# Kernel tuning notes

Measured on AMD Instinct MI355X. Metric: run time of the kernel, lower is better.

## Reference

```python
import jax, jax.numpy as jnp
import numpy as np

B, T, D, H, E = 32, 512, 768, 12, 6  # batch, seq(=input_size), n_embd, num_heads, per-head dim
DFF = 4 * D
EPS = 1e-5


def setup_inputs() -> dict:
    key = jax.random.key(0)
    ks = jax.random.split(key, 10)
    s = 0.02
    return {
        "x": jax.random.normal(ks[0], (B, T, D), jnp.float32),
        "Wq": jax.random.normal(ks[1], (H, D, E), jnp.float32) * s,
        "Wk": jax.random.normal(ks[2], (H, D, E), jnp.float32) * s,
        "Wv": jax.random.normal(ks[3], (H, D, E), jnp.float32) * s,
        "Wo": jax.random.normal(ks[4], (H * E, D), jnp.float32) * s,
        "bo": jnp.zeros((D,), jnp.float32),
        "W1": jax.random.normal(ks[5], (D, DFF), jnp.float32) * s,
        "b1": jnp.zeros((DFF,), jnp.float32),
        "W2": jax.random.normal(ks[6], (DFF, D), jnp.float32) * s,
        "b2": jnp.zeros((D,), jnp.float32),
        "g1": jnp.ones((D,), jnp.float32),
        "beta1": jnp.zeros((D,), jnp.float32),
        "g2": jnp.ones((D,), jnp.float32),
        "beta2": jnp.zeros((D,), jnp.float32),
    }


def _layernorm(x, g, b):
    m = jnp.mean(x, axis=-1, keepdims=True)
    v = jnp.var(x, axis=-1, keepdims=True)  # biased, matches torch LayerNorm
    return (x - m) * jax.lax.rsqrt(v + EPS) * g + b


def reference(x, Wq, Wk, Wv, Wo, bo, W1, b1, W2, b2, g1, beta1, g2, beta2):
    # --- pre-LN multi-head causal attention (dropout = identity, eval mode) ---
    xn = _layernorm(x, g1, beta1)
    q = jnp.einsum("btd,hde->bhte", xn, Wq)
    k = jnp.einsum("btd,hde->bhte", xn, Wk)
    v = jnp.einsum("btd,hde->bhte", xn, Wv)
    scores = jnp.einsum("bhte,bhse->bhts", q, k) * (E ** -0.5)
    causal = jnp.tril(jnp.ones((T, T), dtype=bool))
    scores = jnp.where(causal, scores, -jnp.inf)
    w = jax.nn.softmax(scores, axis=-1)
    o = jnp.einsum("bhts,bhse->bhte", w, v)
    o = o.transpose(0, 2, 1, 3).reshape(B, T, H * E)  # concat heads -> [B,T,72]
    x = x + o @ Wo + bo
    # --- pre-LN feed-forward ---
    y = _layernorm(x, g2, beta2)
    ff = jax.nn.relu(y @ W1 + b1) @ W2 + b2
    return x + ff
```

## Files before the change

### kernel.cpp

```cpp
#include <hip/hip_runtime.h>
#include <hip/hip_bf16.h>

#define BT 16384
#define DIM 768
#define NH 12
#define DFF 3072

typedef __attribute__((ext_vector_type(8))) short short8;
typedef __attribute__((ext_vector_type(4))) float floatx4;
typedef __attribute__((ext_vector_type(4))) unsigned short ushort4b;

using bf16 = __hip_bfloat16;

static __device__ __forceinline__ float b2f(bf16 v) { return __bfloat162float(v); }
static __device__ __forceinline__ bf16 f2b(float v) { return __float2bfloat16(v); }

static __device__ __forceinline__ void gload_lds16(const void* g, void* l) {
    __builtin_amdgcn_global_load_lds(
        (const __attribute__((address_space(1))) unsigned int*)g,
        (__attribute__((address_space(3))) unsigned int*)l, 16, 0, 0);
}

__global__ __launch_bounds__(256) void pack_small_kernel(
    const float* __restrict__ Wq, const float* __restrict__ Wk, const float* __restrict__ Wv,
    const float* __restrict__ Wo, bf16* __restrict__ wqkv, bf16* __restrict__ wo_t)
{
    int i = blockIdx.x * 256 + threadIdx.x;
    const int S0 = 256 * 768, S1 = 768 * 96;
    if (i < S0) {
        int c = i / 768, dd = i % 768;
        float v = 0.f;
        if (c < 216) {
            int sel = c / 72, cc = c % 72, h = cc / 6, e = cc % 6;
            const float* W = (sel == 0) ? Wq : (sel == 1) ? Wk : Wv;
            v = W[((size_t)h * 768 + dd) * 6 + e];
        }
        wqkv[i] = f2b(v);
    } else if ((i -= S0) < S1) {
        int n = i / 96, r = i % 96;
        wo_t[i] = f2b(r < 72 ? Wo[r * 768 + n] : 0.f);
    }
}

__global__ __launch_bounds__(256) void transpose_kernel(
    const float* __restrict__ in, bf16* __restrict__ out, int R, int C)
{
    __shared__ float t[32][33];
    int c0 = blockIdx.x * 32, r0 = blockIdx.y * 32;
    int cx = threadIdx.x & 31, ry = threadIdx.x >> 5;
#pragma unroll
    for (int j = 0; j < 4; j++)
        t[ry + j * 8][cx] = in[(size_t)(r0 + ry + j * 8) * C + c0 + cx];
    __syncthreads();
    int rx = cx, cy = ry;
#pragma unroll
    for (int j = 0; j < 4; j++)
        out[(size_t)(c0 + cy + j * 8) * R + r0 + rx] = f2b(t[rx][cy + j * 8]);
}

__global__ __launch_bounds__(192) void ln_kernel(
    const float* __restrict__ x, const float* __restrict__ g, const float* __restrict__ be,
    bf16* __restrict__ out)
{
    int row = blockIdx.x;
    int tid = threadIdx.x;
    const float4* xr = (const float4*)(x + (size_t)row * DIM);
    float4 v = xr[tid];
    float s = v.x + v.y + v.z + v.w;
    float s2 = v.x * v.x + v.y * v.y + v.z * v.z + v.w * v.w;
#pragma unroll
    for (int off = 32; off; off >>= 1) {
        s += __shfl_down(s, off);
        s2 += __shfl_down(s2, off);
    }
    __shared__ float red[6];
    int wv = tid >> 6, ln = tid & 63;
    if (ln == 0) { red[wv] = s; red[3 + wv] = s2; }
    __syncthreads();
    float ts = red[0] + red[1] + red[2];
    float ts2 = red[3] + red[4] + red[5];
    float mean = ts * (1.f / 768.f);
    float var = ts2 * (1.f / 768.f) - mean * mean;
    float rstd = rsqrtf(var + 1e-5f);
    int c = tid * 4;
    float o0 = (v.x - mean) * rstd * g[c + 0] + be[c + 0];
    float o1 = (v.y - mean) * rstd * g[c + 1] + be[c + 1];
    float o2 = (v.z - mean) * rstd * g[c + 2] + be[c + 2];
    float o3 = (v.w - mean) * rstd * g[c + 3] + be[c + 3];
    bf16 h0 = f2b(o0), h1 = f2b(o1), h2 = f2b(o2), h3 = f2b(o3);
    ushort4b pk;
    pk[0] = *(unsigned short*)&h0; pk[1] = *(unsigned short*)&h1;
    pk[2] = *(unsigned short*)&h2; pk[3] = *(unsigned short*)&h3;
    *(ushort4b*)(out + (size_t)row * DIM + c) = pk;
}

template <int NSLAB, bool RELU, bool BIAS, bool RES, bool BF16OUT>
__global__ __launch_bounds__(256) void gemm_kernel(
    const bf16* __restrict__ A, const bf16* __restrict__ Bt,
    const float* __restrict__ bias, const float* __restrict__ res,
    void* __restrict__ Cv, int M, int N, int K)
{
    constexpr int SMEM_BYTES = BF16OUT ? (128 * 136 * 2) : (NSLAB * 2 * 128 * 32 * 2);
    __shared__ __align__(16) char smem[SMEM_BYTES];
    bf16* lA = (bf16*)smem;
    bf16* lB = lA + NSLAB * 128 * 32;

    const int tid = threadIdx.x;
    const int bm = blockIdx.x * 128;
    const int bn = blockIdx.y * 128;
    const int wave = tid >> 6, lane = tid & 63;
    const int wm = (wave >> 1) * 64, wn = (wave & 1) * 64;
    const int quad = lane >> 4, l16 = lane & 15;
    const int lrow = lane >> 2;
    const int lkc = (lane & 3) * 8;

    floatx4 acc[4][4] = {};

    for (int k0 = 0; k0 < K; k0 += NSLAB * 32) {
#pragma unroll
        for (int s = 0; s < NSLAB; s++) {
#pragma unroll
            for (int it = 0; it < 2; it++) {
                int r = wave * 32 + it * 16;
                gload_lds16(A + (size_t)(bm + r + lrow) * K + k0 + s * 32 + lkc,
                            lA + s * 4096 + r * 32);
                gload_lds16(Bt + (size_t)(bn + r + lrow) * K + k0 + s * 32 + lkc,
                            lB + s * 4096 + r * 32);
            }
        }
        __syncthreads();
#pragma unroll
        for (int s = 0; s < NSLAB; s++) {
            short8 af[4], bfr[4];
#pragma unroll
            for (int mt = 0; mt < 4; mt++)
                af[mt] = *(const short8*)(lA + s * 4096 + (wm + mt * 16 + l16) * 32 + quad * 8);
#pragma unroll
            for (int nt = 0; nt < 4; nt++)
                bfr[nt] = *(const short8*)(lB + s * 4096 + (wn + nt * 16 + l16) * 32 + quad * 8);
#pragma unroll
            for (int mt = 0; mt < 4; mt++)
#pragma unroll
                for (int nt = 0; nt < 4; nt++)
                    acc[mt][nt] = __builtin_amdgcn_mfma_f32_16x16x32_bf16(af[mt], bfr[nt], acc[mt][nt], 0, 0, 0);
        }
        __syncthreads();
    }

    if constexpr (BF16OUT) {
        bf16* ltile = (bf16*)smem;
#pragma unroll
        for (int mt = 0; mt < 4; mt++) {
#pragma unroll
            for (int nt = 0; nt < 4; nt++) {
                int tc = wn + nt * 16 + l16;
#pragma unroll
                for (int r = 0; r < 4; r++) {
                    int tr = wm + mt * 16 + quad * 4 + r;
                    float v0 = acc[mt][nt][r];
                    if constexpr (BIAS) v0 += bias[bn + tc];
                    if constexpr (RELU) v0 = fmaxf(v0, 0.f);
                    ltile[tr * 136 + tc] = f2b(v0);
                }
            }
        }
        __syncthreads();
        bf16* C = (bf16*)Cv;
        int rr0 = tid >> 4, col8 = (tid & 15) * 8;
        int gc = bn + col8;
#pragma unroll
        for (int p = 0; p < 8; p++) {
            int rr = p * 16 + rr0;
            if (gc < N)
                *(short8*)(C + (size_t)(bm + rr) * N + gc) =
                    *(const short8*)(ltile + rr * 136 + col8);
        }
    } else {
        float* C = (float*)Cv;
#pragma unroll
        for (int mt = 0; mt < 4; mt++) {
#pragma unroll
            for (int nt = 0; nt < 4; nt++) {
                int gc = bn + wn + nt * 16 + l16;
                if (gc < N) {
#pragma unroll
                    for (int r = 0; r < 4; r++) {
                        int gr = bm + wm + mt * 16 + quad * 4 + r;
                        float v0 = acc[mt][nt][r];
                        if constexpr (BIAS) v0 += bias[gc];
                        if constexpr (RES) v0 += res[(size_t)gr * N + gc];
                        if constexpr (RELU) v0 = fmaxf(v0, 0.f);
                        C[(size_t)gr * N + gc] = v0;
                    }
                }
            }
        }
    }
}

template <int NTC, int TPB, bool RELU, bool BIAS, bool RES, bool BF16OUT>
__global__ __launch_bounds__(512, 2) void gemm192_kernel(
    const bf16* __restrict__ A, const bf16* __restrict__ Bt,
    const float* __restrict__ bias, const float* __restrict__ res,
    void* __restrict__ Cv, int N)
{
    constexpr int KC = NTC * 64;
    constexpr int NG = NTC * TPB;
    extern __shared__ __align__(16) char smem[];

    const int sid = ((blockIdx.x & 7) << 5) + (blockIdx.x >> 3);
    const int bm = (sid & 63) << 8;
    const int bnBase = (sid >> 6) * (TPB * 192);

    const int tid = threadIdx.x;
    const int w = tid >> 6, lane = tid & 63;
    const int wm = w >> 1, wn = w & 1;
    const int l16 = lane & 15, quad = lane >> 4;

    const int rstg = (w >> 1) * 16 + (lane >> 2);
    const int cstg = (w & 1) * 32 + (((lane & 3) * 8) ^ ((lane & 32) ? 16 : 0));
    const bf16* aSrc = A + (size_t)(bm + rstg) * KC + cstg;
    const bf16* bSrc = Bt + (size_t)(bnBase + rstg) * KC + cstg;
    const int stgoff = w * 1024;

    const int xr = (quad * 16) ^ ((l16 & 8) ? 32 : 0);
    const int aoff = wm * 8192 + l16 * 64 + xr;
    const int boff = 32768 + wn * 12288 + l16 * 64 + xr;

#define STG2(BO, ISB, CH) gload_lds16( \
        ((ISB) ? bS2 : aS2) + (size_t)(CH) * 64 * KC, \
        smem + (BO) + (ISB) * 32768 + (CH) * 8192 + stgoff)

#define BARX() asm volatile("s_barrier" ::: "memory")
#define VMW(N_) asm volatile("s_waitcnt vmcnt(" #N_ ")" ::: "memory")
#define LGW0() asm volatile("s_waitcnt lgkmcnt(0)" ::: "memory")

    floatx4 acc[4][6] = {};
    short8 a[2][2][2], b[2][3][2];

#define LDA(QM, CB) { _Pragma("unroll") for (int fm = 0; fm < 2; fm++) { \
    _Pragma("unroll") for (int s = 0; s < 2; s++) \
        a[QM][fm][s] = *(const short8*)((CB) + aoff + (QM) * 4096 + fm * 2048 + s * 1024); } }
#define LDB(QN, CB) { _Pragma("unroll") for (int fn = 0; fn < 3; fn++) { \
    _Pragma("unroll") for (int s = 0; s < 2; s++) \
        b[QN][fn][s] = *(const short8*)((CB) + boff + (QN) * 6144 + fn * 2048 + s * 1024); } }
#define MM(QM, QN) { __builtin_amdgcn_s_setprio(1); \
    _Pragma("unroll") for (int fm = 0; fm < 2; fm++) { \
    _Pragma("unroll") for (int fn = 0; fn < 3; fn++) { \
    _Pragma("unroll") for (int s = 0; s < 2; s++) \
        acc[(QM)*2+fm][(QN)*3+fn] = __builtin_amdgcn_mfma_f32_16x16x32_bf16( \
            a[QM][fm][s], b[(QN)][fn][s], acc[(QM)*2+fm][(QN)*3+fn], 0, 0, 0); } } \
    __builtin_amdgcn_s_setprio(0); }

    {
        const bf16* aS2 = aSrc;           const bf16* bS2 = bSrc;
#pragma unroll
        for (int c = 0; c < 4; c++) STG2(0, 0, c);
#pragma unroll
        for (int c = 0; c < 3; c++) STG2(0, 1, c);
        aS2 = aSrc + 64; bS2 = bSrc + 64;
#pragma unroll
        for (int c = 0; c < 4; c++) STG2(57344, 0, c);
#pragma unroll
        for (int c = 0; c < 3; c++) STG2(57344, 1, c);
    }
    VMW(7);
    BARX();
    LDA(0, smem); LDB(0, smem);

    for (int G = 0; G < NG; ++G) {
        const int bo = (G & 1) * 57344;
        const char* cb = smem + bo;
        const char* nb = smem + (bo ^ 57344);
        const int v = G + 2;
        const bf16* aS2 = aSrc;
        const bf16* bS2 = bSrc;
        if (v < NG) {
            const int t2 = v / NTC, g2 = v - t2 * NTC;
            aS2 = aSrc + (size_t)g2 * 64;
            bS2 = bSrc + (size_t)t2 * (192 * (size_t)KC) + (size_t)g2 * 64;
        }
        LDA(1, cb);
        MM(0, 0);
        BARX();
        LDB(1, cb);
        MM(1, 0);
        VMW(0);
        BARX();
        if (v < NG) { STG2(bo, 0, 0); STG2(bo, 0, 1); STG2(bo, 0, 2); STG2(bo, 0, 3); }
        if (G + 1 < NG) LDB(0, nb);
        MM(1, 1);
        BARX();
        if (v < NG) { STG2(bo, 1, 0); STG2(bo, 1, 1); STG2(bo, 1, 2); }
        MM(0, 1);
        if (G + 1 < NG) LDA(0, nb);
        BARX();

        if constexpr (BF16OUT) {
            if ((G % NTC) == NTC - 1) {
                const int t = G / NTC;
                const int bnt = bnBase + t * 192;
                bf16* sc = (bf16*)(smem + 114688);
                bf16* C = (bf16*)Cv;
#pragma unroll
                for (int ci = 0; ci < 4; ci++) {
                    if (wn == (ci >> 1)) {
                        const int nfh = ci & 1;
#pragma unroll
                        for (int mf = 0; mf < 4; mf++) {
#pragma unroll
                            for (int n3 = 0; n3 < 3; n3++) {
                                const int nf = nfh * 3 + n3;
                                const int row = wm * 64 + mf * 16 + quad * 4;
                                float bv = BIAS ? bias[bnt + wn * 96 + nf * 16 + l16] : 0.f;
#pragma unroll
                                for (int r = 0; r < 4; r++) {
                                    float vv = acc[mf][nf][r] + bv;
                                    if constexpr (RELU) vv = fmaxf(vv, 0.f);
                                    sc[(row + r) * 56 + n3 * 16 + l16] = f2b(vv);
                                }
                            }
                        }
                    }
                    LGW0();
                    BARX();
#pragma unroll
                    for (int it = 0; it < 3; it++) {
                        int c = it * 512 + tid;
                        int rr = c / 6, cc = (c - rr * 6) * 8;
                        *(short8*)(C + (size_t)(bm + rr) * N + bnt + ci * 48 + cc) =
                            *(const short8*)(sc + rr * 56 + cc);
                    }
                    BARX();
                }
#pragma unroll
                for (int mf = 0; mf < 4; mf++)
#pragma unroll
                    for (int nf = 0; nf < 6; nf++)
                        acc[mf][nf] = (floatx4){0.f, 0.f, 0.f, 0.f};
            }
        }
    }

    if constexpr (!BF16OUT) {
        float* C = (float*)Cv;
        const int bn = bnBase;
#pragma unroll
        for (int mf = 0; mf < 4; mf++) {
            const int gr = bm + wm * 64 + mf * 16 + quad * 4;
#pragma unroll
            for (int nf = 0; nf < 6; nf++) {
                const int gc = bn + wn * 96 + nf * 16 + l16;
                float bv = BIAS ? bias[gc] : 0.f;
#pragma unroll
                for (int r = 0; r < 4; r++) {
                    float v = acc[mf][nf][r] + bv;
                    if constexpr (RES) v += res[(size_t)(gr + r) * N + gc];
                    if constexpr (RELU) v = fmaxf(v, 0.f);
                    C[(size_t)(gr + r) * N + gc] = v;
                }
            }
        }
    }
#undef STG2
#undef BARX
#undef VMW
#undef LGW0
#undef LDA
#undef LDB
#undef MM
}

__global__ __launch_bounds__(256) void attn_kernel(const bf16* __restrict__ qkv, bf16* __restrict__ o_pad)
{
    int blk = blockIdx.x;
    int half = blk & 1;
    int bh = blk >> 1;
    int b = bh / NH, h = bh % NH;
    int wave = threadIdx.x >> 6, lane = threadIdx.x & 63;
    const int jmap0[4] = {0, 2, 5, 7}, jmap1[4] = {1, 3, 4, 6};
    int j = half ? jmap1[wave] : jmap0[wave];
    int t = j * 64 + lane;
    int smax = half ? 448 : 512;

    __shared__ float ks[512 * 6];
    __shared__ float vs[512 * 6];
    const bf16* base = qkv + (size_t)b * 512 * 216;
    for (int i = threadIdx.x; i < smax * 6; i += 256) {
        int s = i / 6, e = i % 6;
        ks[i] = b2f(base[s * 216 + 72 + h * 6 + e]);
        vs[i] = b2f(base[s * 216 + 144 + h * 6 + e]);
    }
    __syncthreads();

    float q0 = b2f(base[t * 216 + h * 6 + 0]);
    float q1 = b2f(base[t * 216 + h * 6 + 1]);
    float q2 = b2f(base[t * 216 + h * 6 + 2]);
    float q3 = b2f(base[t * 216 + h * 6 + 3]);
    float q4 = b2f(base[t * 216 + h * 6 + 4]);
    float q5 = b2f(base[t * 216 + h * 6 + 5]);

    const float scale = 0.4082482904638630f;
    float m = -1e30f, l = 0.f;
    float o0 = 0, o1 = 0, o2 = 0, o3 = 0, o4 = 0, o5 = 0;
    for (int s = 0; s <= t; s++) {
        const float* kk = &ks[s * 6];
        float sc = (q0 * kk[0] + q1 * kk[1] + q2 * kk[2] + q3 * kk[3] + q4 * kk[4] + q5 * kk[5]) * scale;
        float nm = fmaxf(m, sc);
        float alpha = __expf(m - nm);
        float p = __expf(sc - nm);
        l = l * alpha + p;
        const float* vv = &vs[s * 6];
        o0 = o0 * alpha + p * vv[0];
        o1 = o1 * alpha + p * vv[1];
        o2 = o2 * alpha + p * vv[2];
        o3 = o3 * alpha + p * vv[3];
        o4 = o4 * alpha + p * vv[4];
        o5 = o5 * alpha + p * vv[5];
        m = nm;
    }
    float inv = 1.f / l;
    bf16* orow = o_pad + (size_t)(b * 512 + t) * 96 + h * 6;
    orow[0] = f2b(o0 * inv);
    orow[1] = f2b(o1 * inv);
    orow[2] = f2b(o2 * inv);
    orow[3] = f2b(o3 * inv);
    orow[4] = f2b(o4 * inv);
    orow[5] = f2b(o5 * inv);
}

extern "C" void kernel_launch(void* const* d_in, const int* in_sizes, int n_in,
                              void* d_out, int out_size, void* d_ws, size_t ws_size,
                              hipStream_t stream)
{
    const float* x   = (const float*)d_in[0];
    const float* Wq  = (const float*)d_in[1];
    const float* Wk  = (const float*)d_in[2];
    const float* Wv  = (const float*)d_in[3];
    const float* Wo  = (const float*)d_in[4];
    const float* bo  = (const float*)d_in[5];
    const float* W1  = (const float*)d_in[6];
    const float* b1  = (const float*)d_in[7];
    const float* W2  = (const float*)d_in[8];
    const float* b2  = (const float*)d_in[9];
    const float* g1  = (const float*)d_in[10];
    const float* be1 = (const float*)d_in[11];
    const float* g2  = (const float*)d_in[12];
    const float* be2 = (const float*)d_in[13];

    char* ws = (char*)d_ws;
    size_t off = 0;
    auto alloc = [&](size_t bytes) {
        void* p = ws + off;
        off = (off + bytes + 255) & ~(size_t)255;
        return p;
    };
    bf16*  xn    = (bf16*)alloc((size_t)BT * DIM * 2);
    bf16*  qkvb  = (bf16*)alloc((size_t)BT * 216 * 2);
    bf16*  o_pad = (bf16*)alloc((size_t)BT * 96 * 2);
    float* x1    = (float*)alloc((size_t)BT * DIM * 4);
    bf16*  ffb   = (bf16*)alloc((size_t)BT * DFF * 2);
    bf16*  wqkv  = (bf16*)alloc((size_t)256 * 768 * 2);
    bf16*  wo_t  = (bf16*)alloc((size_t)768 * 96 * 2);
    bf16*  w1t   = (bf16*)alloc((size_t)3072 * 768 * 2);
    bf16*  w2t   = (bf16*)alloc((size_t)768 * 3072 * 2);

    hipFuncSetAttribute(reinterpret_cast<const void*>(&gemm192_kernel<12, 4, true, true, false, true>),
                        hipFuncAttributeMaxDynamicSharedMemorySize, 143360);
    hipFuncSetAttribute(reinterpret_cast<const void*>(&gemm192_kernel<48, 1, false, true, true, false>),
                        hipFuncAttributeMaxDynamicSharedMemorySize, 114688);

    const int PACK_N = 256 * 768 + 768 * 96;
    pack_small_kernel<<<(PACK_N + 255) / 256, 256, 0, stream>>>(Wq, Wk, Wv, Wo, wqkv, wo_t);
    transpose_kernel<<<dim3(3072 / 32, 768 / 32), 256, 0, stream>>>(W1, w1t, 768, 3072);
    transpose_kernel<<<dim3(768 / 32, 3072 / 32), 256, 0, stream>>>(W2, w2t, 3072, 768);

    ln_kernel<<<BT, 192, 0, stream>>>(x, g1, be1, xn);
    gemm_kernel<2, false, false, false, true><<<dim3(128, 2), 256, 0, stream>>>(
        xn, wqkv, nullptr, nullptr, qkvb, BT, 216, 768);
    attn_kernel<<<32 * NH * 2, 256, 0, stream>>>(qkvb, o_pad);
    gemm_kernel<1, false, true, true, false><<<dim3(128, 6), 256, 0, stream>>>(
        o_pad, wo_t, bo, x, x1, BT, 768, 96);
    ln_kernel<<<BT, 192, 0, stream>>>(x1, g2, be2, xn);
    gemm192_kernel<12, 4, true, true, false, true><<<256, 512, 143360, stream>>>(
        xn, w1t, b1, nullptr, ffb, 3072);
    gemm192_kernel<48, 1, false, true, true, false><<<256, 512, 114688, stream>>>(
        ffb, w2t, b2, x1, (float*)d_out, 768);
}
```

Baseline: 443.9 us.

## Add 256x256-tile GEMM for FFN up-projection and remap block swizzle

Introduces a new gemm256 kernel with 256x256 output tiles, an 8-wave 2x4 layout, double-buffered LDS staging and a full-tile bf16 epilogue through LDS. It replaces the persistent 192-wide gemm192 kernel for the W1 GEMM, using 768 blocks instead of 256. The per-tile BF16 epilogue is removed from gemm192, and its block-to-tile swizzle is changed for the W2 GEMM. The aim is more data reuse per tile and better L2 locality, at the cost of heavier register and LDS use (143 KB per block).

```diff
diff --git a/kernel.cpp b/kernel.cpp
--- a/kernel.cpp
+++ b/kernel.cpp
@@ -198,6 +198,135 @@
     }
 }
 
+template <bool RELU, bool BIAS, bool RES, bool BF16OUT>
+__global__ __launch_bounds__(512, 2) void gemm256_kernel(
+    const bf16* __restrict__ A, const bf16* __restrict__ Bt,
+    const float* __restrict__ bias, const float* __restrict__ res,
+    void* __restrict__ Cv, int M, int N, int K)
+{
+    extern __shared__ __align__(16) char smem[];
+    const int NT = K >> 6;
+    const int k8 = blockIdx.x & 7, q = blockIdx.x >> 3;
+    const int bm = (k8 * 8 + (q & 7)) << 8;
+    const int bn = (q >> 3) << 8;
+
+    const int tid = threadIdx.x;
+    const int w = tid >> 6, lane = tid & 63;
+    const int wm = w >> 2, wn = w & 3;
+    const int l16 = lane & 15, quad = lane >> 4;
+
+    const int rstg = (w >> 1) * 16 + (lane >> 2);
+    const int cstg = (w & 1) * 32 + ((((lane & 3) * 8)) ^ ((lane & 32) ? 16 : 0));
+    const bf16* aSrc = A + (size_t)(bm + rstg) * K + cstg;
+    const bf16* bSrc = Bt + (size_t)(bn + rstg) * K + cstg;
+    char* dstBase = smem + w * 1024;
+
+    const int xr = (quad * 16) ^ ((l16 & 8) ? 32 : 0);
+    const int aOff = wm * 16384 + l16 * 64 + xr;
+    const int bOff = 32768 + wn * 8192 + l16 * 64 + xr;
+
+#define STAGE(P, ISB, H, T) { \
+    const bf16* _s = ((ISB) ? bSrc : aSrc) + ((size_t)((H) * 128) * K + (size_t)(T) * 64); \
+    char* _d = dstBase + (P) * 65536 + (ISB) * 32768 + (H) * 16384; \
+    gload_lds16(_s, _d); \
+    gload_lds16(_s + (size_t)64 * K, _d + 8192); }
+
+#define BARX() asm volatile("s_barrier" ::: "memory")
+#define VMW(N_) asm volatile("s_waitcnt vmcnt(" #N_ ")" ::: "memory")
+
+    floatx4 acc[8][4] = {};
+    short8 a[4][2], b[2][2][2];
+
+#define LDA(QM, CB) { _Pragma("unroll") for (int fm = 0; fm < 4; fm++) { \
+    _Pragma("unroll") for (int s = 0; s < 2; s++) \
+        a[fm][s] = *(const short8*)((CB) + aOff + (QM) * 8192 + fm * 2048 + s * 1024); } }
+#define LDB(QN, CB) { _Pragma("unroll") for (int fn = 0; fn < 2; fn++) { \
+    _Pragma("unroll") for (int s = 0; s < 2; s++) \
+        b[QN][fn][s] = *(const short8*)((CB) + bOff + (QN) * 4096 + fn * 2048 + s * 1024); } }
+#define MM(QM, QN) { __builtin_amdgcn_s_setprio(1); \
+    _Pragma("unroll") for (int fm = 0; fm < 4; fm++) { \
+    _Pragma("unroll") for (int fn = 0; fn < 2; fn++) { \
+    _Pragma("unroll") for (int s = 0; s < 2; s++) \
+        acc[(QM)*4+fm][(QN)*2+fn] = __builtin_amdgcn_mfma_f32_16x16x32_bf16( \
+            a[fm][s], b[QN][fn][s], acc[(QM)*4+fm][(QN)*2+fn], 0, 0, 0); } } \
+    __builtin_amdgcn_s_setprio(0); }
+
+    STAGE(0, 1, 0, 0); STAGE(0, 1, 1, 0); STAGE(0, 0, 0, 0); STAGE(0, 0, 1, 0);
+    STAGE(1, 1, 0, 1); STAGE(1, 1, 1, 1); STAGE(1, 0, 0, 1);
+    VMW(6);
+    BARX();
+
+    for (int g = 0; g < NT; ++g) {
+        const int p = g & 1, pn = p ^ 1;
+        const char* cb = smem + p * 65536;
+        LDA(0, cb); LDB(0, cb);
+        if (g + 1 < NT) STAGE(pn, 0, 1, g + 1);
+        BARX(); MM(0, 0); BARX();
+        LDB(1, cb);
+        BARX(); MM(0, 1); BARX();
+        LDA(1, cb);
+        if (g + 2 < NT) STAGE(p, 1, 0, g + 2);
+        BARX(); MM(1, 0); BARX();
+        if (g + 2 < NT) { STAGE(p, 1, 1, g + 2); STAGE(p, 0, 0, g + 2); }
+        BARX(); MM(1, 1);
+        if (g < NT - 2) { VMW(6); } else { VMW(0); }
+        BARX();
+    }
+
+    if constexpr (BF16OUT) {
+        bf16* lt = (bf16*)smem;
+#pragma unroll
+        for (int RF = 0; RF < 8; RF++) {
+            const int row = wm * 128 + (RF >> 2) * 64 + (RF & 3) * 16 + quad * 4;
+#pragma unroll
+            for (int CF = 0; CF < 4; CF++) {
+                const int col = wn * 64 + (CF >> 1) * 32 + (CF & 1) * 16 + l16;
+                float bv = BIAS ? bias[bn + col] : 0.f;
+#pragma unroll
+                for (int rr = 0; rr < 4; rr++) {
+                    float v = acc[RF][CF][rr] + bv;
+                    if constexpr (RELU) v = fmaxf(v, 0.f);
+                    lt[(row + rr) * 280 + col] = f2b(v);
+                }
+            }
+        }
+        asm volatile("s_waitcnt lgkmcnt(0)" ::: "memory");
+        BARX();
+        bf16* C = (bf16*)Cv;
+#pragma unroll
+        for (int it = 0; it < 16; it++) {
+            int c = it * 512 + tid;
+            int rr = c >> 5, c8 = (c & 31) * 8;
+            *(short8*)(C + (size_t)(bm + rr) * N + bn + c8) =
+                *(const short8*)(lt + rr * 280 + c8);
+        }
+    } else {
+        float* C = (float*)Cv;
+#pragma unroll
+        for (int RF = 0; RF < 8; RF++) {
+            const int gr = bm + wm * 128 + (RF >> 2) * 64 + (RF & 3) * 16 + quad * 4;
+#pragma unroll
+            for (int CF = 0; CF < 4; CF++) {
+                const int gc = bn + wn * 64 + (CF >> 1) * 32 + (CF & 1) * 16 + l16;
+                float bv = BIAS ? bias[gc] : 0.f;
+#pragma unroll
+                for (int rr = 0; rr < 4; rr++) {
+                    float v = acc[RF][CF][rr] + bv;
+                    if constexpr (RES) v += res[(size_t)(gr + rr) * N + gc];
+                    if constexpr (RELU) v = fmaxf(v, 0.f);
+                    C[(size_t)(gr + rr) * N + gc] = v;
+                }
+            }
+        }
+    }
+#undef STAGE
+#undef BARX
+#undef VMW
+#undef LDA
+#undef LDB
+#undef MM
+}
+
 template <int NTC, int TPB, bool RELU, bool BIAS, bool RES, bool BF16OUT>
 __global__ __launch_bounds__(512, 2) void gemm192_kernel(
     const bf16* __restrict__ A, const bf16* __restrict__ Bt,
@@ -208,7 +337,8 @@
     constexpr int NG = NTC * TPB;
     extern __shared__ __align__(16) char smem[];
 
-    const int sid = ((blockIdx.x & 7) << 5) + (blockIdx.x >> 3);
+    const int k8 = blockIdx.x & 7, q = blockIdx.x >> 3;
+    const int sid = (q >> 3) * 64 + k8 * 8 + (q & 7);
     const int bm = (sid & 63) << 8;
     const int bnBase = (sid >> 6) * (TPB * 192);
 
@@ -295,51 +425,6 @@
         MM(0, 1);
         if (G + 1 < NG) LDA(0, nb);
         BARX();
-
-        if constexpr (BF16OUT) {
-            if ((G % NTC) == NTC - 1) {
-                const int t = G / NTC;
-                const int bnt = bnBase + t * 192;
-                bf16* sc = (bf16*)(smem + 114688);
-                bf16* C = (bf16*)Cv;
-#pragma unroll
-                for (int ci = 0; ci < 4; ci++) {
-                    if (wn == (ci >> 1)) {
-                        const int nfh = ci & 1;
-#pragma unroll
-                        for (int mf = 0; mf < 4; mf++) {
-#pragma unroll
-                            for (int n3 = 0; n3 < 3; n3++) {
-                                const int nf = nfh * 3 + n3;
-                                const int row = wm * 64 + mf * 16 + quad * 4;
-                                float bv = BIAS ? bias[bnt + wn * 96 + nf * 16 + l16] : 0.f;
-#pragma unroll
-                                for (int r = 0; r < 4; r++) {
-                                    float vv = acc[mf][nf][r] + bv;
-                                    if constexpr (RELU) vv = fmaxf(vv, 0.f);
-                                    sc[(row + r) * 56 + n3 * 16 + l16] = f2b(vv);
-                                }
-                            }
-                        }
-                    }
-                    LGW0();
-                    BARX();
-#pragma unroll
-                    for (int it = 0; it < 3; it++) {
-                        int c = it * 512 + tid;
-                        int rr = c / 6, cc = (c - rr * 6) * 8;
-                        *(short8*)(C + (size_t)(bm + rr) * N + bnt + ci * 48 + cc) =
-                            *(const short8*)(sc + rr * 56 + cc);
-                    }
-                    BARX();
-                }
-#pragma unroll
-                for (int mf = 0; mf < 4; mf++)
-#pragma unroll
-                    for (int nf = 0; nf < 6; nf++)
-                        acc[mf][nf] = (floatx4){0.f, 0.f, 0.f, 0.f};
-            }
-        }
     }
 
     if constexpr (!BF16OUT) {
@@ -465,8 +550,8 @@
     bf16*  w1t   = (bf16*)alloc((size_t)3072 * 768 * 2);
     bf16*  w2t   = (bf16*)alloc((size_t)768 * 3072 * 2);
 
-    hipFuncSetAttribute(reinterpret_cast<const void*>(&gemm192_kernel<12, 4, true, true, false, true>),
-                        hipFuncAttributeMaxDynamicSharedMemorySize, 143360);
+    hipFuncSetAttribute(reinterpret_cast<const void*>(&gemm256_kernel<true, true, false, true>),
+                        hipFuncAttributeMaxDynamicSharedMemorySize, 256 * 280 * 2);
     hipFuncSetAttribute(reinterpret_cast<const void*>(&gemm192_kernel<48, 1, false, true, true, false>),
                         hipFuncAttributeMaxDynamicSharedMemorySize, 114688);
 
@@ -482,8 +567,8 @@
     gemm_kernel<1, false, true, true, false><<<dim3(128, 6), 256, 0, stream>>>(
         o_pad, wo_t, bo, x, x1, BT, 768, 96);
     ln_kernel<<<BT, 192, 0, stream>>>(x1, g2, be2, xn);
-    gemm192_kernel<12, 4, true, true, false, true><<<256, 512, 143360, stream>>>(
-        xn, w1t, b1, nullptr, ffb, 3072);
+    gemm256_kernel<true, true, false, true><<<768, 512, 256 * 280 * 2, stream>>>(
+        xn, w1t, b1, nullptr, ffb, BT, 3072, 768);
     gemm192_kernel<48, 1, false, true, true, false><<<256, 512, 114688, stream>>>(
         ffb, w2t, b2, x1, (float*)d_out, 768);
 }
```

Result: faster. 414.8 us (-6.6%).
